# Kernel tuning notes

Hardware: AMD Instinct MI355X
Metric: run time of the kernel (lower is better)

## Reference

```python
import jax, jax.numpy as jnp
import numpy as np

B, T, C, H = 2, 2048, 1024, 16
HS = C // H  # head_size = 64
EPS = 1e-5


def _layernorm(x, w, b):
    mu = jnp.mean(x, axis=-1, keepdims=True)
    var = jnp.mean(jnp.square(x - mu), axis=-1, keepdims=True)
    return (x - mu) * jax.lax.rsqrt(var + EPS) * w + b


def setup_inputs() -> dict:
    key = jax.random.key(0)
    ks = jax.random.split(key, 12)
    s_attn = 1.0 / np.sqrt(C)
    s_ff1 = 1.0 / np.sqrt(C)
    s_ff2 = 1.0 / np.sqrt(4 * C)
    return {
        "x": jax.random.normal(ks[0], (B, T, C), dtype=jnp.float32),
        "ln1_w": jnp.ones((C,), jnp.float32),
        "ln1_b": jnp.zeros((C,), jnp.float32),
        "Wq": jax.random.normal(ks[1], (H, C, HS), jnp.float32) * s_attn,
        "Wk": jax.random.normal(ks[2], (H, C, HS), jnp.float32) * s_attn,
        "Wv": jax.random.normal(ks[3], (H, C, HS), jnp.float32) * s_attn,
        "proj_w": jax.random.normal(ks[4], (C, C), jnp.float32) * s_attn,
        "proj_b": jnp.zeros((C,), jnp.float32),
        "ln2_w": jnp.ones((C,), jnp.float32),
        "ln2_b": jnp.zeros((C,), jnp.float32),
        "fc1_w": jax.random.normal(ks[5], (C, 4 * C), jnp.float32) * s_ff1,
        "fc1_b": jnp.zeros((4 * C,), jnp.float32),
        "fc2_w": jax.random.normal(ks[6], (4 * C, C), jnp.float32) * s_ff2,
        "fc2_b": jnp.zeros((C,), jnp.float32),
    }


def reference(x, ln1_w, ln1_b, Wq, Wk, Wv, proj_w, proj_b, ln2_w, ln2_b, fc1_w, fc1_b, fc2_w, fc2_b):
    Bx, Tx, Cx = x.shape
    # --- self-attention with pre-norm residual ---
    h = _layernorm(x, ln1_w, ln1_b)                       # [B,T,C]
    q = jnp.einsum("btc,hcd->bhtd", h, Wq)                 # [B,H,T,HS]
    k = jnp.einsum("btc,hcd->bhtd", h, Wk)
    v = jnp.einsum("btc,hcd->bhtd", h, Wv)
    # NOTE: original code applies NO 1/sqrt(d) scaling -- keep faithful.
    wei = jnp.einsum("bhtd,bhsd->bhts", q, k)              # [B,H,T,T]
    causal = jnp.tril(jnp.ones((Tx, Tx), dtype=bool))
    wei = jnp.where(causal, wei, -jnp.inf)
    wei = jax.nn.softmax(wei, axis=-1)
    attn = jnp.einsum("bhts,bhsd->bhtd", wei, v)           # [B,H,T,HS]
    attn = attn.transpose(0, 2, 1, 3).reshape(Bx, Tx, Cx)  # concat heads
    sa = attn @ proj_w + proj_b                            # output projection
    x = x + sa
    # --- FFN with pre-norm residual ---
    h2 = _layernorm(x, ln2_w, ln2_b)
    ff = jax.nn.relu(h2 @ fc1_w + fc1_b) @ fc2_w + fc2_b
    return x + ff
```

## Files before the change

kernel.cpp:

```cpp
#include <hip/hip_runtime.h>
#include <hip/hip_bf16.h>

#define Bn 2
#define Tn 2048
#define Cn 1024
#define Hn 16
#define HSn 64
#define Mn (Bn*Tn)
#define LN_EPS 1e-5f

typedef unsigned short u16;
typedef __attribute__((ext_vector_type(8))) short bf16x8;
typedef __attribute__((ext_vector_type(4))) float f32x4;

#define MFMA16(a,b,c) __builtin_amdgcn_mfma_f32_16x16x32_bf16(a, b, c, 0, 0, 0)
#define GLL16(g,l) __builtin_amdgcn_global_load_lds( \
    (const __attribute__((address_space(1))) void*)(g), \
    (__attribute__((address_space(3))) void*)(l), 16, 0, 0)

__device__ __forceinline__ u16 f2b(float f) {
    unsigned int u = __float_as_uint(f);
    unsigned int r = (u + 0x7FFFu + ((u >> 16) & 1u)) >> 16;
    return (u16)r;
}

__global__ __launch_bounds__(256) void wqkv_t(
    const float* __restrict__ Wq, const float* __restrict__ Wk,
    const float* __restrict__ Wv, u16* __restrict__ Wt)
{
    int z = blockIdx.z, h = blockIdx.y, c0 = blockIdx.x * 64;
    const float* in = (z == 0 ? Wq : z == 1 ? Wk : Wv) + (size_t)h * 65536;
    __shared__ float t[64][68];
    int tid = threadIdx.x;
#pragma unroll
    for (int it = 0; it < 4; it++) {
        int r = it * 16 + (tid >> 4);
        *(float4*)&t[r][(tid & 15) * 4] =
            *(const float4*)(in + (size_t)(c0 + r) * 64 + (tid & 15) * 4);
    }
    __syncthreads();
    int d = tid >> 2, seg = tid & 3;
    union { u16 u[8]; uint4 q; } pk;
#pragma unroll
    for (int hq = 0; hq < 2; hq++) {
#pragma unroll
        for (int j = 0; j < 8; j++) pk.u[j] = f2b(t[seg * 16 + hq * 8 + j][d]);
        *(uint4*)(Wt + (size_t)(z * 1024 + h * 64 + d) * 1024 + c0 + seg * 16 + hq * 8) = pk.q;
    }
}

__global__ __launch_bounds__(256) void transpose_cvt(
    const float* __restrict__ in, u16* __restrict__ out, int R, int C)
{
    __shared__ float t[64][68];
    int r0 = blockIdx.y * 64, c0 = blockIdx.x * 64;
    int tid = threadIdx.x;
#pragma unroll
    for (int it = 0; it < 4; it++) {
        int r = it * 16 + (tid >> 4);
        *(float4*)&t[r][(tid & 15) * 4] =
            *(const float4*)(in + (size_t)(r0 + r) * C + c0 + (tid & 15) * 4);
    }
    __syncthreads();
    int c = tid >> 2, seg = tid & 3;
    union { u16 u[8]; uint4 q; } pk;
#pragma unroll
    for (int hq = 0; hq < 2; hq++) {
#pragma unroll
        for (int j = 0; j < 8; j++) pk.u[j] = f2b(t[seg * 16 + hq * 8 + j][c]);
        *(uint4*)(out + (size_t)(c0 + c) * R + r0 + seg * 16 + hq * 8) = pk.q;
    }
}

__global__ __launch_bounds__(256) void ln_bf16(
    const float* __restrict__ x, const float* __restrict__ w,
    const float* __restrict__ bvec, u16* __restrict__ out)
{
    int row  = blockIdx.x * 4 + (threadIdx.x >> 6);
    int lane = threadIdx.x & 63;
    const float* xr = x + (size_t)row * Cn;
    float4 v[4];
    float s = 0.f, sq = 0.f;
#pragma unroll
    for (int i = 0; i < 4; i++) {
        v[i] = *(const float4*)(xr + lane * 4 + i * 256);
        s  += v[i].x + v[i].y + v[i].z + v[i].w;
        sq += v[i].x * v[i].x + v[i].y * v[i].y + v[i].z * v[i].z + v[i].w * v[i].w;
    }
#pragma unroll
    for (int off = 1; off < 64; off <<= 1) {
        s  += __shfl_xor(s, off);
        sq += __shfl_xor(sq, off);
    }
    float mu   = s * (1.f / Cn);
    float var  = sq * (1.f / Cn) - mu * mu;
    float rstd = rsqrtf(var + LN_EPS);
    u16* orow = out + (size_t)row * Cn;
#pragma unroll
    for (int i = 0; i < 4; i++) {
        float4 w4 = *(const float4*)(w    + lane * 4 + i * 256);
        float4 b4 = *(const float4*)(bvec + lane * 4 + i * 256);
        union { u16 u[4]; uint2 q; } pk;
        pk.u[0] = f2b((v[i].x - mu) * rstd * w4.x + b4.x);
        pk.u[1] = f2b((v[i].y - mu) * rstd * w4.y + b4.y);
        pk.u[2] = f2b((v[i].z - mu) * rstd * w4.z + b4.z);
        pk.u[3] = f2b((v[i].w - mu) * rstd * w4.w + b4.w);
        *(uint2*)(orow + lane * 4 + i * 256) = pk.q;
    }
}

template<int OBF, int BIAS, int RELU>
__global__ __launch_bounds__(512, 2) void gemm_8ph(
    const u16* __restrict__ A, const u16* __restrict__ Bt,
    const float* __restrict__ bias, void* Cout,
    int M, int N, int K, int NT)
{
    __shared__ u16 lds[65536];
    const int tid = threadIdx.x, l = tid & 63, w = tid >> 6;
    const int wm = w >> 2, wn = w & 3;
    const int g = l >> 4, c16 = l & 15;

    const int nwg = (int)gridDim.x, cpx = nwg >> 3;
    const int bid = (int)blockIdx.x;
    const int sbid = (bid & 7) * cpx + (bid >> 3);
    const int m0 = (sbid / NT) * 256, n0 = (sbid % NT) * 256;

    const int sr = tid >> 3;
    const int ss = ((tid & 7) ^ (sr & 7)) << 3;
    const u16* Asrc = A  + (size_t)(m0 + sr) * K + ss;
    const u16* Bsrc = Bt + (size_t)(n0 + sr) * K + ss;
    const int dst0 = tid * 8;

#define ST_A8(d_, h_, kt_) do {                                              \
        GLL16(Asrc + (size_t)((h_) * 128) * K + (size_t)(kt_) * 64,          \
              &lds[(d_) * 32768 + (h_) * 8192 + dst0]);                      \
        GLL16(Asrc + (size_t)((h_) * 128 + 64) * K + (size_t)(kt_) * 64,     \
              &lds[(d_) * 32768 + (h_) * 8192 + 4096 + dst0]);               \
    } while (0)
#define ST_B8(d_, h_, kt_) do {                                              \
        GLL16(Bsrc + (size_t)((h_) * 128) * K + (size_t)(kt_) * 64,          \
              &lds[(d_) * 32768 + 16384 + (h_) * 8192 + dst0]);              \
        GLL16(Bsrc + (size_t)((h_) * 128 + 64) * K + (size_t)(kt_) * 64,     \
              &lds[(d_) * 32768 + 16384 + (h_) * 8192 + 4096 + dst0]);       \
    } while (0)
#define LDA8(d_, mi_, s_) (*(const bf16x8*)&lds[(d_) * 32768 +               \
        (wm * 128 + (mi_) * 16 + c16) * 64 +                                  \
        ((((s_) * 4 + g) ^ ((wm * 128 + (mi_) * 16 + c16) & 7)) << 3)])
#define LDB8(d_, nj_, s_) (*(const bf16x8*)&lds[(d_) * 32768 + 16384 +       \
        (wn * 64 + (nj_) * 16 + c16) * 64 +                                   \
        ((((s_) * 4 + g) ^ ((wn * 64 + (nj_) * 16 + c16) & 7)) << 3)])
#define PH_HEAD() do {                                                       \
        __builtin_amdgcn_s_barrier();                                        \
        asm volatile("s_waitcnt lgkmcnt(0)" ::: "memory");                   \
        __builtin_amdgcn_sched_barrier(0);                                   \
        __builtin_amdgcn_s_setprio(1);                                       \
    } while (0)
#define PH_MFMA(NH_) do {                                                    \
        _Pragma("unroll")                                                    \
        for (int mi = 0; mi < 8; mi++) {                                     \
            acc[mi][2*(NH_)]   = MFMA16(aF[mi], bF[0], acc[mi][2*(NH_)]);    \
            acc[mi][2*(NH_)+1] = MFMA16(aF[mi], bF[1], acc[mi][2*(NH_)+1]);  \
        }                                                                    \
    } while (0)

    f32x4 acc[8][4];
#pragma unroll
    for (int i = 0; i < 8; i++)
#pragma unroll
        for (int j = 0; j < 4; j++) acc[i][j] = (f32x4){0.f, 0.f, 0.f, 0.f};

    const int nk = K >> 6;
    ST_A8(0, 0, 0); ST_A8(0, 1, 0); ST_B8(0, 0, 0); ST_B8(0, 1, 0);
    ST_A8(1, 0, 1); ST_A8(1, 1, 1);
    asm volatile("s_waitcnt vmcnt(4)" ::: "memory");
    __builtin_amdgcn_s_barrier();

    bf16x8 aF[8], bF[2];
    for (int m = 0; m < nk; m++) {
        const int d = m & 1, dn = d ^ 1;
#pragma unroll
        for (int mi = 0; mi < 8; mi++) aF[mi] = LDA8(d, mi, 0);
        bF[0] = LDB8(d, 0, 0); bF[1] = LDB8(d, 1, 0);
        if (m + 1 < nk) ST_B8(dn, 0, m + 1);
        PH_HEAD(); PH_MFMA(0);
        __builtin_amdgcn_s_setprio(0);
        __builtin_amdgcn_s_barrier();
        bF[0] = LDB8(d, 2, 0); bF[1] = LDB8(d, 3, 0);
        if (m + 1 < nk) ST_B8(dn, 1, m + 1);
        PH_HEAD(); PH_MFMA(1);
        __builtin_amdgcn_s_setprio(0);
        __builtin_amdgcn_s_barrier();
#pragma unroll
        for (int mi = 0; mi < 8; mi++) aF[mi] = LDA8(d, mi, 1);
        bF[0] = LDB8(d, 0, 1); bF[1] = LDB8(d, 1, 1);
        PH_HEAD(); PH_MFMA(0);
        __builtin_amdgcn_s_setprio(0);
        __builtin_amdgcn_s_barrier();
        bF[0] = LDB8(d, 2, 1); bF[1] = LDB8(d, 3, 1);
        if (m + 2 < nk) { ST_A8(d, 0, m + 2); ST_A8(d, 1, m + 2); }
        PH_HEAD(); PH_MFMA(1);
        __builtin_amdgcn_s_setprio(0);
        if (m + 1 < nk) {
            if (m + 2 < nk) asm volatile("s_waitcnt vmcnt(4)" ::: "memory");
            else            asm volatile("s_waitcnt vmcnt(0)" ::: "memory");
        }
        __builtin_amdgcn_s_barrier();
    }
#undef ST_A8
#undef ST_B8
#undef LDA8
#undef LDB8
#undef PH_HEAD
#undef PH_MFMA

#pragma unroll
    for (int mi = 0; mi < 8; mi++)
#pragma unroll
        for (int nj = 0; nj < 4; nj++) {
            const int coln = n0 + wn * 64 + nj * 16 + c16;
            float bv = BIAS ? bias[coln] : 0.f;
#pragma unroll
            for (int reg = 0; reg < 4; reg++) {
                int rowm = m0 + wm * 128 + mi * 16 + 4 * g + reg;
                float v = acc[mi][nj][reg] + bv;
                if (RELU) v = fmaxf(v, 0.f);
                if (OBF) ((u16*)Cout)[(size_t)rowm * N + coln] = f2b(v);
                else     ((float*)Cout)[(size_t)rowm * N + coln] = v;
            }
        }
}

__global__ __launch_bounds__(512, 2) void gemm_fc2(
    const u16* __restrict__ A, const u16* __restrict__ Bt,
    const float* __restrict__ bias, float* __restrict__ out,
    float* __restrict__ part)
{
    __shared__ u16 lds[65536];
    const int tid = threadIdx.x, l = tid & 63, w = tid >> 6;
    const int wm = w >> 2, wn = w & 3;
    const int g = l >> 4, c16 = l & 15;

    const int bid = (int)blockIdx.x;
    const int sbid = (bid & 7) * 32 + (bid >> 3);
    const int chunk = sbid >> 6, t = sbid & 63;
    const int m0 = (t >> 2) * 256, n0 = (t & 3) * 256;
    const int kB = chunk << 10;

    const int sr = tid >> 3;
    const int ss = ((tid & 7) ^ (sr & 7)) << 3;
    const u16* Asrc = A  + (size_t)(m0 + sr) * 4096 + kB + ss;
    const u16* Bsrc = Bt + (size_t)(n0 + sr) * 4096 + kB + ss;
    const int dst0 = tid * 8;

#define ST_A8(d_, h_, kt_) do {                                              \
        GLL16(Asrc + (size_t)((h_) * 128) * 4096 + (size_t)(kt_) * 64,       \
              &lds[(d_) * 32768 + (h_) * 8192 + dst0]);                      \
        GLL16(Asrc + (size_t)((h_) * 128 + 64) * 4096 + (size_t)(kt_) * 64,  \
              &lds[(d_) * 32768 + (h_) * 8192 + 4096 + dst0]);               \
    } while (0)
#define ST_B8(d_, h_, kt_) do {                                              \
        GLL16(Bsrc + (size_t)((h_) * 128) * 4096 + (size_t)(kt_) * 64,       \
              &lds[(d_) * 32768 + 16384 + (h_) * 8192 + dst0]);              \
        GLL16(Bsrc + (size_t)((h_) * 128 + 64) * 4096 + (size_t)(kt_) * 64,  \
              &lds[(d_) * 32768 + 16384 + (h_) * 8192 + 4096 + dst0]);       \
    } while (0)
#define LDA8(d_, mi_, s_) (*(const bf16x8*)&lds[(d_) * 32768 +               \
        (wm * 128 + (mi_) * 16 + c16) * 64 +                                  \
        ((((s_) * 4 + g) ^ ((wm * 128 + (mi_) * 16 + c16) & 7)) << 3)])
#define LDB8(d_, nj_, s_) (*(const bf16x8*)&lds[(d_) * 32768 + 16384 +       \
        (wn * 64 + (nj_) * 16 + c16) * 64 +                                   \
        ((((s_) * 4 + g) ^ ((wn * 64 + (nj_) * 16 + c16) & 7)) << 3)])
#define PH_HEAD() do {                                                       \
        __builtin_amdgcn_s_barrier();                                        \
        asm volatile("s_waitcnt lgkmcnt(0)" ::: "memory");                   \
        __builtin_amdgcn_sched_barrier(0);                                   \
        __builtin_amdgcn_s_setprio(1);                                       \
    } while (0)
#define PH_MFMA(NH_) do {                                                    \
        _Pragma("unroll")                                                    \
        for (int mi = 0; mi < 8; mi++) {                                     \
            acc[mi][2*(NH_)]   = MFMA16(aF[mi], bF[0], acc[mi][2*(NH_)]);    \
            acc[mi][2*(NH_)+1] = MFMA16(aF[mi], bF[1], acc[mi][2*(NH_)+1]);  \
        }                                                                    \
    } while (0)

    f32x4 acc[8][4];
#pragma unroll
    for (int i = 0; i < 8; i++)
#pragma unroll
        for (int j = 0; j < 4; j++) acc[i][j] = (f32x4){0.f, 0.f, 0.f, 0.f};

    const int nk = 16;
    ST_A8(0, 0, 0); ST_A8(0, 1, 0); ST_B8(0, 0, 0); ST_B8(0, 1, 0);
    ST_A8(1, 0, 1); ST_A8(1, 1, 1);
    asm volatile("s_waitcnt vmcnt(4)" ::: "memory");
    __builtin_amdgcn_s_barrier();

    bf16x8 aF[8], bF[2];
    for (int m = 0; m < nk; m++) {
        const int d = m & 1, dn = d ^ 1;
#pragma unroll
        for (int mi = 0; mi < 8; mi++) aF[mi] = LDA8(d, mi, 0);
        bF[0] = LDB8(d, 0, 0); bF[1] = LDB8(d, 1, 0);
        if (m + 1 < nk) ST_B8(dn, 0, m + 1);
        PH_HEAD(); PH_MFMA(0);
        __builtin_amdgcn_s_setprio(0);
        __builtin_amdgcn_s_barrier();
        bF[0] = LDB8(d, 2, 0); bF[1] = LDB8(d, 3, 0);
        if (m + 1 < nk) ST_B8(dn, 1, m + 1);
        PH_HEAD(); PH_MFMA(1);
        __builtin_amdgcn_s_setprio(0);
        __builtin_amdgcn_s_barrier();
#pragma unroll
        for (int mi = 0; mi < 8; mi++) aF[mi] = LDA8(d, mi, 1);
        bF[0] = LDB8(d, 0, 1); bF[1] = LDB8(d, 1, 1);
        PH_HEAD(); PH_MFMA(0);
        __builtin_amdgcn_s_setprio(0);
        __builtin_amdgcn_s_barrier();
        bF[0] = LDB8(d, 2, 1); bF[1] = LDB8(d, 3, 1);
        if (m + 2 < nk) { ST_A8(d, 0, m + 2); ST_A8(d, 1, m + 2); }
        PH_HEAD(); PH_MFMA(1);
        __builtin_amdgcn_s_setprio(0);
        if (m + 1 < nk) {
            if (m + 2 < nk) asm volatile("s_waitcnt vmcnt(4)" ::: "memory");
            else            asm volatile("s_waitcnt vmcnt(0)" ::: "memory");
        }
        __builtin_amdgcn_s_barrier();
    }
#undef ST_A8
#undef ST_B8
#undef LDA8
#undef LDB8
#undef PH_HEAD
#undef PH_MFMA

    if (chunk == 0) {
#pragma unroll
        for (int mi = 0; mi < 8; mi++)
#pragma unroll
            for (int nj = 0; nj < 4; nj++) {
                const int coln = n0 + wn * 64 + nj * 16 + c16;
                float bv = bias[coln];
#pragma unroll
                for (int reg = 0; reg < 4; reg++) {
                    int rowm = m0 + wm * 128 + mi * 16 + 4 * g + reg;
                    size_t idx = (size_t)rowm * 1024 + coln;
                    out[idx] = acc[mi][nj][reg] + bv + out[idx];
                }
            }
    } else {
        float* pp = part + (size_t)(chunk - 1) * 4194304;
#pragma unroll
        for (int mi = 0; mi < 8; mi++)
#pragma unroll
            for (int nj = 0; nj < 4; nj++) {
                const int coln = n0 + wn * 64 + nj * 16 + c16;
#pragma unroll
                for (int reg = 0; reg < 4; reg++) {
                    int rowm = m0 + wm * 128 + mi * 16 + 4 * g + reg;
                    pp[(size_t)rowm * 1024 + coln] = acc[mi][nj][reg];
                }
            }
    }
}

__global__ __launch_bounds__(256) void splitk_reduce(
    const float* __restrict__ part, float* __restrict__ out)
{
    size_t i = ((size_t)blockIdx.x * 256 + threadIdx.x) * 4;
    float4 o = *(float4*)(out + i);
    float4 a = *(const float4*)(part + i);
    float4 b = *(const float4*)(part + 4194304 + i);
    float4 c = *(const float4*)(part + 8388608 + i);
    o.x += a.x + b.x + c.x;
    o.y += a.y + b.y + c.y;
    o.z += a.z + b.z + c.z;
    o.w += a.w + b.w + c.w;
    *(float4*)(out + i) = o;
}

template<int OBF, int BIAS, int RES, int RELU>
__global__ __launch_bounds__(256) void gemm_n64(
    const u16* __restrict__ A, const u16* __restrict__ Bt,
    const float* __restrict__ bias, const float* res,
    void* Cout, int M, int N, int K)
{
    __shared__ u16 As[2][8192];
    __shared__ u16 Bs[2][4096];
    const int tid = threadIdx.x;
    const int l = tid & 63, w = tid >> 6;
    const int wr = w >> 1, wc = w & 1;
    const int g = l >> 4, c16 = l & 15;
    const int m0 = blockIdx.y * 128, n0 = blockIdx.x * 64;

    const u16* a_src[4];
    int a_dst[4];
#pragma unroll
    for (int i = 0; i < 4; i++) {
        int G = tid + 256 * i, r = G >> 3, sl = G & 7;
        a_src[i] = A + (size_t)(m0 + r) * K + ((sl ^ (r & 7)) << 3);
        a_dst[i] = G * 8;
    }
    const u16* b_src[2];
    int b_dst[2];
#pragma unroll
    for (int i = 0; i < 2; i++) {
        int G = tid + 256 * i, r = G >> 3, sl = G & 7;
        b_src[i] = Bt + (size_t)(n0 + r) * K + ((sl ^ (r & 7)) << 3);
        b_dst[i] = G * 8;
    }

    f32x4 acc[4][2];
#pragma unroll
    for (int i = 0; i < 4; i++)
#pragma unroll
        for (int j = 0; j < 2; j++) acc[i][j] = (f32x4){0.f, 0.f, 0.f, 0.f};

#define STAGE_N64(nb, k0) do {                                   \
        GLL16(a_src[0] + (k0), &As[nb][a_dst[0]]);               \
        GLL16(a_src[1] + (k0), &As[nb][a_dst[1]]);               \
        GLL16(a_src[2] + (k0), &As[nb][a_dst[2]]);               \
        GLL16(a_src[3] + (k0), &As[nb][a_dst[3]]);               \
        GLL16(b_src[0] + (k0), &Bs[nb][b_dst[0]]);               \
        GLL16(b_src[1] + (k0), &Bs[nb][b_dst[1]]);               \
    } while (0)

    STAGE_N64(0, 0);
    __syncthreads();

    int cur = 0;
    for (int k0 = 0; k0 < K; k0 += 64) {
        if (k0 + 64 < K) STAGE_N64(cur ^ 1, k0 + 64);
        const u16* AsC = As[cur];
        const u16* BsC = Bs[cur];
        bf16x8 af[4][2], bfr[2][2];
#pragma unroll
        for (int fi = 0; fi < 4; fi++) {
            int r = wr * 64 + fi * 16 + c16;
            af[fi][0] = *(const bf16x8*)&AsC[r * 64 + (((g    ) ^ (r & 7)) << 3)];
            af[fi][1] = *(const bf16x8*)&AsC[r * 64 + (((4 + g) ^ (r & 7)) << 3)];
        }
#pragma unroll
        for (int fj = 0; fj < 2; fj++) {
            int r = wc * 32 + fj * 16 + c16;
            bfr[fj][0] = *(const bf16x8*)&BsC[r * 64 + (((g    ) ^ (r & 7)) << 3)];
            bfr[fj][1] = *(const bf16x8*)&BsC[r * 64 + (((4 + g) ^ (r & 7)) << 3)];
        }
#pragma unroll
        for (int fi = 0; fi < 4; fi++)
#pragma unroll
            for (int fj = 0; fj < 2; fj++) {
                acc[fi][fj] = MFMA16(af[fi][0], bfr[fj][0], acc[fi][fj]);
                acc[fi][fj] = MFMA16(af[fi][1], bfr[fj][1], acc[fi][fj]);
            }
        __syncthreads();
        cur ^= 1;
    }
#undef STAGE_N64

#pragma unroll
    for (int fi = 0; fi < 4; fi++)
#pragma unroll
        for (int fj = 0; fj < 2; fj++) {
            int coln = n0 + wc * 32 + fj * 16 + c16;
            float bv = BIAS ? bias[coln] : 0.f;
#pragma unroll
            for (int reg = 0; reg < 4; reg++) {
                int rowm = m0 + wr * 64 + fi * 16 + 4 * g + reg;
                float v = acc[fi][fj][reg] + bv;
                if (RES) v += res[(size_t)rowm * N + coln];
                if (RELU) v = fmaxf(v, 0.f);
                if (OBF) ((u16*)Cout)[(size_t)rowm * N + coln] = f2b(v);
                else     ((float*)Cout)[(size_t)rowm * N + coln] = v;
            }
        }
}

__global__ __launch_bounds__(256) void v_transpose(
    const u16* __restrict__ qkv, u16* __restrict__ vT)
{
    int t0 = blockIdx.x * 64, h = blockIdx.y, b = blockIdx.z;
    __shared__ u16 t[64][72];
    int tid = threadIdx.x;
#pragma unroll
    for (int it = 0; it < 2; it++) {
        int r = it * 32 + (tid >> 3);
        int cs = (tid & 7) * 8;
        *(uint4*)&t[r][cs] =
            *(const uint4*)(qkv + (size_t)(b * 2048 + t0 + r) * 3072 + 2048 + h * 64 + cs);
    }
    __syncthreads();
    int d = tid >> 2, seg = tid & 3;
    union { u16 u[8]; uint4 q; } pk;
#pragma unroll
    for (int hq = 0; hq < 2; hq++) {
#pragma unroll
        for (int j = 0; j < 8; j++) pk.u[j] = t[seg * 16 + hq * 8 + j][d];
        *(uint4*)(vT + (size_t)((b * 16 + h) * 64 + d) * 2048 + t0 + seg * 16 + hq * 8) = pk.q;
    }
}

__global__ __launch_bounds__(512) void attn_mfma(
    const u16* __restrict__ qkv, const u16* __restrict__ vT,
    u16* __restrict__ outb)
{
    __shared__ u16 Ks[2][4096];
    __shared__ u16 Vs[2][4096];
    __shared__ u16 Ps[128 * 72];
    const int tid = threadIdx.x, l = tid & 63, w = tid >> 6;
    const int g = l >> 4, c16 = l & 15;
    const int qt = 15 - (int)blockIdx.x;
    const int bh = blockIdx.y, b = bh >> 4, h = bh & 15;
    const int r0 = qt * 128;
    const int wrow = r0 + w * 16;

    const u16* qrow = qkv + (size_t)(b * 2048 + wrow + c16) * 3072 + h * 64;
    bf16x8 qf0 = *(const bf16x8*)(qrow + g * 8);
    bf16x8 qf1 = *(const bf16x8*)(qrow + 32 + g * 8);

    const int kr = tid >> 3, ks = (tid & 7) ^ (kr & 7);
    const u16* kg = qkv + (size_t)(b * 2048) * 3072 + 1024 + h * 64;
    const u16* vg = vT + (size_t)((b * 16 + h) * 64) * 2048;

    float lrow = 0.f;
    f32x4 oacc[4];
#pragma unroll
    for (int i = 0; i < 4; i++) oacc[i] = (f32x4){0.f, 0.f, 0.f, 0.f};

    const int prow = (w * 16 + c16) * 72;

#define STAGE_KV(nb, s0) do {                                            \
        GLL16(kg + (size_t)((s0) + kr) * 3072 + ks * 8, &Ks[nb][tid * 8]); \
        GLL16(vg + (size_t)kr * 2048 + (s0) + ks * 8, &Vs[nb][tid * 8]);   \
    } while (0)

    STAGE_KV(0, 0);
    __syncthreads();

    const int nt = 2 * qt + 2;
    int cur = 0;
    for (int kt = 0; kt < nt; kt++) {
        if (kt + 1 < nt) STAGE_KV(cur ^ 1, (kt + 1) * 64);
        const u16* KsC = Ks[cur];
        const u16* VsC = Vs[cur];
        const int s0 = kt * 64;

        f32x4 sc[4];
#pragma unroll
        for (int fj = 0; fj < 4; fj++) sc[fj] = (f32x4){0.f, 0.f, 0.f, 0.f};
#pragma unroll
        for (int fj = 0; fj < 4; fj++) {
            int r = fj * 16 + c16;
            bf16x8 kf0 = *(const bf16x8*)&KsC[r * 64 + ((g       ^ (r & 7)) << 3)];
            bf16x8 kf1 = *(const bf16x8*)&KsC[r * 64 + (((4 + g) ^ (r & 7)) << 3)];
            sc[fj] = MFMA16(kf0, qf0, sc[fj]);
            sc[fj] = MFMA16(kf1, qf1, sc[fj]);
        }
        if (s0 + 63 > wrow) {
            const int qg = wrow + c16;
#pragma unroll
            for (int fj = 0; fj < 4; fj++)
#pragma unroll
                for (int reg = 0; reg < 4; reg++)
                    if (s0 + fj * 16 + 4 * g + reg > qg) sc[fj][reg] = -1e30f;
        }
#pragma unroll
        for (int fj = 0; fj < 4; fj++) {
            float p0 = __expf(sc[fj][0]);
            float p1 = __expf(sc[fj][1]);
            float p2 = __expf(sc[fj][2]);
            float p3 = __expf(sc[fj][3]);
            lrow += (p0 + p1) + (p2 + p3);
            uint2 pk;
            pk.x = (unsigned)f2b(p0) | ((unsigned)f2b(p1) << 16);
            pk.y = (unsigned)f2b(p2) | ((unsigned)f2b(p3) << 16);
            *(uint2*)&Ps[prow + fj * 16 + 4 * g] = pk;
        }
#pragma unroll
        for (int kc = 0; kc < 2; kc++) {
            bf16x8 pa = *(const bf16x8*)&Ps[prow + kc * 32 + 8 * g];
#pragma unroll
            for (int fd = 0; fd < 4; fd++) {
                int r = fd * 16 + c16;
                bf16x8 vf = *(const bf16x8*)&VsC[r * 64 + (((4 * kc + g) ^ (r & 7)) << 3)];
                oacc[fd] = MFMA16(pa, vf, oacc[fd]);
            }
        }
        __syncthreads();
        cur ^= 1;
    }
#undef STAGE_KV

    lrow += __shfl_xor(lrow, 16);
    lrow += __shfl_xor(lrow, 32);
#pragma unroll
    for (int reg = 0; reg < 4; reg++) {
        float ls = __shfl(lrow, 4 * g + reg);
        float inv = 1.0f / ls;
        int t = wrow + 4 * g + reg;
        u16* op = outb + (size_t)(b * 2048 + t) * 1024 + h * 64;
#pragma unroll
        for (int fd = 0; fd < 4; fd++)
            op[fd * 16 + c16] = f2b(oacc[fd][reg] * inv);
    }
}

extern "C" void kernel_launch(void* const* d_in, const int* in_sizes, int n_in,
                              void* d_out, int out_size, void* d_ws, size_t ws_size,
                              hipStream_t stream) {
    const float* x     = (const float*)d_in[0];
    const float* ln1w  = (const float*)d_in[1];
    const float* ln1b  = (const float*)d_in[2];
    const float* Wq    = (const float*)d_in[3];
    const float* Wk    = (const float*)d_in[4];
    const float* Wv    = (const float*)d_in[5];
    const float* projw = (const float*)d_in[6];
    const float* projb = (const float*)d_in[7];
    const float* ln2w  = (const float*)d_in[8];
    const float* ln2b  = (const float*)d_in[9];
    const float* fc1w  = (const float*)d_in[10];
    const float* fc1b  = (const float*)d_in[11];
    const float* fc2w  = (const float*)d_in[12];
    const float* fc2b  = (const float*)d_in[13];
    float* out = (float*)d_out;

    u16* h_bf    = (u16*)d_ws;
    u16* qkv_bf  = h_bf    + 4194304;
    u16* vTb     = qkv_bf  + 12582912;
    u16* attn_bf = vTb     + 4194304;
    u16* ff1_bf  = attn_bf + 4194304;
    u16* WtQKV   = ff1_bf  + 16777216;
    u16* WtP     = WtQKV   + 3145728;
    u16* Wt1     = WtP     + 1048576;
    u16* Wt2     = Wt1     + 4194304;
    float* fc2p = (float*)d_ws;

    wqkv_t<<<dim3(16, 16, 3), 256, 0, stream>>>(Wq, Wk, Wv, WtQKV);
    transpose_cvt<<<dim3(16, 16), 256, 0, stream>>>(projw, WtP, 1024, 1024);
    transpose_cvt<<<dim3(64, 16), 256, 0, stream>>>(fc1w, Wt1, 1024, 4096);
    transpose_cvt<<<dim3(16, 64), 256, 0, stream>>>(fc2w, Wt2, 4096, 1024);

    ln_bf16<<<1024, 256, 0, stream>>>(x, ln1w, ln1b, h_bf);
    gemm_8ph<1, 0, 0><<<dim3(192), 512, 0, stream>>>(
        h_bf, WtQKV, nullptr, qkv_bf, Mn, 3072, 1024, 12);
    v_transpose<<<dim3(32, 16, 2), 256, 0, stream>>>(qkv_bf, vTb);
    attn_mfma<<<dim3(16, 32), 512, 0, stream>>>(qkv_bf, vTb, attn_bf);
    gemm_n64<0, 1, 1, 0><<<dim3(16, 32), 256, 0, stream>>>(
        attn_bf, WtP, projb, x, out, Mn, 1024, 1024);
    ln_bf16<<<1024, 256, 0, stream>>>(out, ln2w, ln2b, h_bf);
    gemm_8ph<1, 1, 1><<<dim3(256), 512, 0, stream>>>(
        h_bf, Wt1, fc1b, ff1_bf, Mn, 4096, 1024, 16);
    gemm_fc2<<<dim3(256), 512, 0, stream>>>(ff1_bf, Wt2, fc2b, out, fc2p);
    splitk_reduce<<<dim3(4096), 256, 0, stream>>>(fc2p, out);
}
```

Measured before the change: 238.5 us.

## Give each attention wave two 16-row query groups and XOR-swizzle the P tile

The attention kernel drops from 8 waves to 4 per block, and each wave now processes 32 query rows as two 16-row groups. K and V fragments read from shared memory are reused across both groups, so fewer LDS reads are needed per MFMA. Each thread now stages two K/V chunks per tile. The padded P buffer is replaced by an unpadded one addressed with an XOR swizzle to avoid bank conflicts. In exchange, register pressure per wave rises and fewer waves per block are available to hide latency.

```diff
diff --git a/kernel.cpp b/kernel.cpp
--- a/kernel.cpp
+++ b/kernel.cpp
@@ -500,38 +500,46 @@
     }
 }
 
-__global__ __launch_bounds__(512) void attn_mfma(
+__global__ __launch_bounds__(256) void attn_mfma(
     const u16* __restrict__ qkv, const u16* __restrict__ vT,
     u16* __restrict__ outb)
 {
     __shared__ u16 Ks[2][4096];
     __shared__ u16 Vs[2][4096];
-    __shared__ u16 Ps[128 * 72];
+    __shared__ u16 Ps[128 * 64];
     const int tid = threadIdx.x, l = tid & 63, w = tid >> 6;
     const int g = l >> 4, c16 = l & 15;
     const int qt = 15 - (int)blockIdx.x;
     const int bh = blockIdx.y, b = bh >> 4, h = bh & 15;
     const int r0 = qt * 128;
-    const int wrow = r0 + w * 16;
-
-    const u16* qrow = qkv + (size_t)(b * 2048 + wrow + c16) * 3072 + h * 64;
-    bf16x8 qf0 = *(const bf16x8*)(qrow + g * 8);
-    bf16x8 qf1 = *(const bf16x8*)(qrow + 32 + g * 8);
+    const int wrow = r0 + w * 32;
+
+    bf16x8 qf[2][2];
+#pragma unroll
+    for (int grp = 0; grp < 2; grp++) {
+        const u16* qrow = qkv + (size_t)(b * 2048 + wrow + grp * 16 + c16) * 3072 + h * 64;
+        qf[grp][0] = *(const bf16x8*)(qrow + g * 8);
+        qf[grp][1] = *(const bf16x8*)(qrow + 32 + g * 8);
+    }
 
     const int kr = tid >> 3, ks = (tid & 7) ^ (kr & 7);
     const u16* kg = qkv + (size_t)(b * 2048) * 3072 + 1024 + h * 64;
     const u16* vg = vT + (size_t)((b * 16 + h) * 64) * 2048;
 
-    float lrow = 0.f;
-    f32x4 oacc[4];
-#pragma unroll
-    for (int i = 0; i < 4; i++) oacc[i] = (f32x4){0.f, 0.f, 0.f, 0.f};
-
-    const int prow = (w * 16 + c16) * 72;
-
-#define STAGE_KV(nb, s0) do {                                            \
-        GLL16(kg + (size_t)((s0) + kr) * 3072 + ks * 8, &Ks[nb][tid * 8]); \
-        GLL16(vg + (size_t)kr * 2048 + (s0) + ks * 8, &Vs[nb][tid * 8]);   \
+    float lrow[2] = {0.f, 0.f};
+    f32x4 oacc[2][4];
+#pragma unroll
+    for (int grp = 0; grp < 2; grp++)
+#pragma unroll
+        for (int i = 0; i < 4; i++) oacc[grp][i] = (f32x4){0.f, 0.f, 0.f, 0.f};
+
+    const int swz = (c16 & 7) << 4;
+
+#define STAGE_KV(nb, s0) do {                                                     \
+        GLL16(kg + (size_t)((s0) + kr) * 3072 + ks * 8, &Ks[nb][tid * 8]);        \
+        GLL16(kg + (size_t)((s0) + kr + 32) * 3072 + ks * 8, &Ks[nb][2048 + tid * 8]); \
+        GLL16(vg + (size_t)kr * 2048 + (s0) + ks * 8, &Vs[nb][tid * 8]);          \
+        GLL16(vg + (size_t)(kr + 32) * 2048 + (s0) + ks * 8, &Vs[nb][2048 + tid * 8]); \
     } while (0)
 
     STAGE_KV(0, 0);
@@ -545,45 +553,60 @@
         const u16* VsC = Vs[cur];
         const int s0 = kt * 64;
 
-        f32x4 sc[4];
-#pragma unroll
-        for (int fj = 0; fj < 4; fj++) sc[fj] = (f32x4){0.f, 0.f, 0.f, 0.f};
+        bf16x8 kf0[4], kf1[4];
 #pragma unroll
         for (int fj = 0; fj < 4; fj++) {
             int r = fj * 16 + c16;
-            bf16x8 kf0 = *(const bf16x8*)&KsC[r * 64 + ((g       ^ (r & 7)) << 3)];
-            bf16x8 kf1 = *(const bf16x8*)&KsC[r * 64 + (((4 + g) ^ (r & 7)) << 3)];
-            sc[fj] = MFMA16(kf0, qf0, sc[fj]);
-            sc[fj] = MFMA16(kf1, qf1, sc[fj]);
-        }
-        if (s0 + 63 > wrow) {
-            const int qg = wrow + c16;
-#pragma unroll
-            for (int fj = 0; fj < 4; fj++)
-#pragma unroll
-                for (int reg = 0; reg < 4; reg++)
-                    if (s0 + fj * 16 + 4 * g + reg > qg) sc[fj][reg] = -1e30f;
-        }
-#pragma unroll
-        for (int fj = 0; fj < 4; fj++) {
-            float p0 = __expf(sc[fj][0]);
-            float p1 = __expf(sc[fj][1]);
-            float p2 = __expf(sc[fj][2]);
-            float p3 = __expf(sc[fj][3]);
-            lrow += (p0 + p1) + (p2 + p3);
-            uint2 pk;
-            pk.x = (unsigned)f2b(p0) | ((unsigned)f2b(p1) << 16);
-            pk.y = (unsigned)f2b(p2) | ((unsigned)f2b(p3) << 16);
-            *(uint2*)&Ps[prow + fj * 16 + 4 * g] = pk;
+            kf0[fj] = *(const bf16x8*)&KsC[r * 64 + ((g       ^ (r & 7)) << 3)];
+            kf1[fj] = *(const bf16x8*)&KsC[r * 64 + (((4 + g) ^ (r & 7)) << 3)];
+        }
+#pragma unroll
+        for (int grp = 0; grp < 2; grp++) {
+            f32x4 sc[4];
+#pragma unroll
+            for (int fj = 0; fj < 4; fj++) sc[fj] = (f32x4){0.f, 0.f, 0.f, 0.f};
+#pragma unroll
+            for (int fj = 0; fj < 4; fj++) {
+                sc[fj] = MFMA16(kf0[fj], qf[grp][0], sc[fj]);
+                sc[fj] = MFMA16(kf1[fj], qf[grp][1], sc[fj]);
+            }
+            const int gbase = wrow + grp * 16;
+            if (s0 + 63 > gbase) {
+                const int qg = gbase + c16;
+#pragma unroll
+                for (int fj = 0; fj < 4; fj++)
+#pragma unroll
+                    for (int reg = 0; reg < 4; reg++)
+                        if (s0 + fj * 16 + 4 * g + reg > qg) sc[fj][reg] = -1e30f;
+            }
+            const int prow = (gbase - r0 + c16) * 64;
+#pragma unroll
+            for (int fj = 0; fj < 4; fj++) {
+                float p0 = __expf(sc[fj][0]);
+                float p1 = __expf(sc[fj][1]);
+                float p2 = __expf(sc[fj][2]);
+                float p3 = __expf(sc[fj][3]);
+                lrow[grp] += (p0 + p1) + (p2 + p3);
+                uint2 pk;
+                pk.x = (unsigned)f2b(p0) | ((unsigned)f2b(p1) << 16);
+                pk.y = (unsigned)f2b(p2) | ((unsigned)f2b(p3) << 16);
+                *(uint2*)((char*)&Ps[prow] + ((fj * 32 + 8 * g) ^ swz)) = pk;
+            }
         }
 #pragma unroll
         for (int kc = 0; kc < 2; kc++) {
-            bf16x8 pa = *(const bf16x8*)&Ps[prow + kc * 32 + 8 * g];
+            bf16x8 pa[2];
+#pragma unroll
+            for (int grp = 0; grp < 2; grp++) {
+                const int prow = (w * 32 + grp * 16 + c16) * 64;
+                pa[grp] = *(const bf16x8*)((char*)&Ps[prow] + ((kc * 64 + 16 * g) ^ swz));
+            }
 #pragma unroll
             for (int fd = 0; fd < 4; fd++) {
                 int r = fd * 16 + c16;
                 bf16x8 vf = *(const bf16x8*)&VsC[r * 64 + (((4 * kc + g) ^ (r & 7)) << 3)];
-                oacc[fd] = MFMA16(pa, vf, oacc[fd]);
+                oacc[0][fd] = MFMA16(pa[0], vf, oacc[0][fd]);
+                oacc[1][fd] = MFMA16(pa[1], vf, oacc[1][fd]);
             }
         }
         __syncthreads();
@@ -591,17 +614,21 @@
     }
 #undef STAGE_KV
 
-    lrow += __shfl_xor(lrow, 16);
-    lrow += __shfl_xor(lrow, 32);
-#pragma unroll
-    for (int reg = 0; reg < 4; reg++) {
-        float ls = __shfl(lrow, 4 * g + reg);
-        float inv = 1.0f / ls;
-        int t = wrow + 4 * g + reg;
-        u16* op = outb + (size_t)(b * 2048 + t) * 1024 + h * 64;
-#pragma unroll
-        for (int fd = 0; fd < 4; fd++)
-            op[fd * 16 + c16] = f2b(oacc[fd][reg] * inv);
+#pragma unroll
+    for (int grp = 0; grp < 2; grp++) {
+        float lr = lrow[grp];
+        lr += __shfl_xor(lr, 16);
+        lr += __shfl_xor(lr, 32);
+#pragma unroll
+        for (int reg = 0; reg < 4; reg++) {
+            float ls = __shfl(lr, 4 * g + reg);
+            float inv = 1.0f / ls;
+            int t = wrow + grp * 16 + 4 * g + reg;
+            u16* op = outb + (size_t)(b * 2048 + t) * 1024 + h * 64;
+#pragma unroll
+            for (int fd = 0; fd < 4; fd++)
+                op[fd * 16 + c16] = f2b(oacc[grp][fd][reg] * inv);
+        }
     }
 }
 
@@ -644,7 +671,7 @@
     gemm_8ph<1, 0, 0><<<dim3(192), 512, 0, stream>>>(
         h_bf, WtQKV, nullptr, qkv_bf, Mn, 3072, 1024, 12);
     v_transpose<<<dim3(32, 16, 2), 256, 0, stream>>>(qkv_bf, vTb);
-    attn_mfma<<<dim3(16, 32), 512, 0, stream>>>(qkv_bf, vTb, attn_bf);
+    attn_mfma<<<dim3(16, 32), 256, 0, stream>>>(qkv_bf, vTb, attn_bf);
     gemm_n64<0, 1, 1, 0><<<dim3(16, 32), 256, 0, stream>>>(
         attn_bf, WtP, projb, x, out, Mn, 1024, 1024);
     ln_bf16<<<1024, 256, 0, stream>>>(out, ln2w, ln2b, h_bf);
```

Result: slower. 249.4 us (+4.6%).
